# Kernel tuning notes

Measured on AMD Instinct MI355X. Metric: run time of the kernel, lower is better.

The kernel has to match this reference:

```python
import jax, jax.numpy as jnp
import numpy as np

# Problem-size constants (match input_specs / init_kwargs)
B, D, H, W = 2, 128, 128, 128   # batch and spatial grid
N = 200_000                      # number of active (non-empty) voxels
CI, CO, K = 64, 64, 3            # channels and cubic kernel size
DIL = 1                          # dilation


def setup_inputs() -> dict:
    key = jax.random.key(0)
    k1, k2, k3 = jax.random.split(key, 3)
    # Unique active voxel coordinates (submanifold conv assumes unique sites).
    rng = np.random.default_rng(0)
    lin = rng.choice(B * D * H * W, size=N, replace=False)
    b, rem = np.divmod(lin, D * H * W)
    z, rem = np.divmod(rem, H * W)
    y, x = np.divmod(rem, W)
    coords = jnp.asarray(np.stack([b, z, y, x], axis=1).astype(np.int32))  # [N,4]
    feats = jax.random.normal(k1, (N, CI), dtype=jnp.float32)
    # kaiming-uniform-ish init, layout [Co, Kd, Kh, Kw, Ci] as in the module
    fan_in = CI * K * K * K
    bound = 1.0 / np.sqrt(fan_in)
    weight = jax.random.uniform(k2, (CO, K, K, K, CI), dtype=jnp.float32,
                                minval=-bound, maxval=bound)
    bias = jax.random.uniform(k3, (CO,), dtype=jnp.float32,
                              minval=-bound, maxval=bound)
    return {"feats": feats, "weight": weight, "bias": bias, "coords": coords}


def _build_grid(coords):
    """Dense voxel hash: linear cell id -> row index in feats (-1 if empty)."""
    n = coords.shape[0]
    lin = ((coords[:, 0] * D + coords[:, 1]) * H + coords[:, 2]) * W + coords[:, 3]
    grid = jnp.full((B * D * H * W,), -1, dtype=jnp.int32)
    return grid.at[lin].set(jnp.arange(n, dtype=jnp.int32))


def reference(feats, weight, bias, coords):
    # Submanifold sparse 3D conv: out[p] = bias + sum_k W[k] @ feats[p + dil*(k - center)]
    # (only where the neighbor voxel is active; output sites == input sites).
    n = feats.shape[0]
    grid = _build_grid(coords)
    c = K // 2
    bz, z0, y0, x0 = coords[:, 0], coords[:, 1], coords[:, 2], coords[:, 3]
    out = jnp.broadcast_to(bias.astype(feats.dtype), (n, CO))
    for kd in range(K):
        for kh in range(K):
            for kw in range(K):
                dz, dy, dx = DIL * (kd - c), DIL * (kh - c), DIL * (kw - c)
                nz, ny, nx = z0 + dz, y0 + dy, x0 + dx
                inb = (nz >= 0) & (nz < D) & (ny >= 0) & (ny < H) & (nx >= 0) & (nx < W)
                nlin = ((bz * D + jnp.clip(nz, 0, D - 1)) * H
                        + jnp.clip(ny, 0, H - 1)) * W + jnp.clip(nx, 0, W - 1)
                nidx = jnp.where(inb, grid[nlin], -1)          # rulebook for this offset
                valid = (nidx >= 0)[:, None]
                g = jnp.where(valid, feats[jnp.clip(nidx, 0)], 0.0)  # gather [N,Ci]
                out = out + jnp.einsum('nc,oc->no', g, weight[:, kd, kh, kw, :])
    return out
```

## Files before the change

### kernel.cpp

```cpp
#include <hip/hip_runtime.h>
#include <hip/hip_bf16.h>

#define BDIM 2
#define DDIM 128
#define HDIM 128
#define WDIM 128
#define CI 64
#define CO 64
#define NTAPS 27
#define GRID_CELLS (BDIM * DDIM * HDIM * WDIM)
#define NCBLK (GRID_CELLS / 256)

typedef __attribute__((ext_vector_type(8))) short short8;
typedef __attribute__((ext_vector_type(4))) float floatx4;

#define WT_OFF   ((size_t)16 << 20)
#define BCNT_OFF (WT_OFF + ((size_t)256 << 10))
#define ORD_OFF  (BCNT_OFF + ((size_t)64 << 10))

__device__ __forceinline__ unsigned short f2bf(float f) {
    unsigned int u = __float_as_uint(f);
    return (unsigned short)((u + 0x7FFFu + ((u >> 16) & 1u)) >> 16);
}

__global__ __launch_bounds__(256) void scatter_kernel(
    const int* __restrict__ coords, int* __restrict__ grid, int n) {
    int i = blockIdx.x * blockDim.x + threadIdx.x;
    if (i >= n) return;
    int4 c = ((const int4*)coords)[i];
    grid[((c.x * DDIM + c.y) * HDIM + c.z) * WDIM + c.w] = i;
}

__global__ __launch_bounds__(256) void wfrag_kernel(
    const float* __restrict__ weight, short8* __restrict__ wt8) {
    int idx = blockIdx.x * blockDim.x + threadIdx.x;
    if (idx >= NTAPS * 2 * 4 * 64) return;
    int l = idx & 63, ot = (idx >> 6) & 3, s = (idx >> 8) & 1, t = idx >> 9;
    int o = ot * 16 + (l & 15);
    int k0 = s * 32 + ((l >> 4) << 3);
    const float* src = weight + ((size_t)o * NTAPS + t) * CI + k0;
    short8 v;
#pragma unroll
    for (int j = 0; j < 8; ++j) v[j] = (short)f2bf(src[j]);
    wt8[idx] = v;
}

__global__ __launch_bounds__(256) void count_kernel(
    const int* __restrict__ grid, int* __restrict__ bcnt) {
    int i = blockIdx.x * 256 + threadIdx.x;
    unsigned long long b = __ballot(grid[i] >= 0);
    __shared__ int wc[4];
    if ((threadIdx.x & 63) == 0) wc[threadIdx.x >> 6] = __popcll(b);
    __syncthreads();
    if (threadIdx.x == 0) bcnt[blockIdx.x] = wc[0] + wc[1] + wc[2] + wc[3];
}

__global__ __launch_bounds__(1024) void scan_kernel(int* __restrict__ bcnt) {
    __shared__ int part[1024];
    int tid = threadIdx.x;
    int v[16], s = 0;
#pragma unroll
    for (int k = 0; k < 16; ++k) { v[k] = bcnt[tid * 16 + k]; s += v[k]; }
    part[tid] = s;
    __syncthreads();
    for (int off = 1; off < 1024; off <<= 1) {
        int t = (tid >= off) ? part[tid - off] : 0;
        __syncthreads();
        part[tid] += t;
        __syncthreads();
    }
    int ex = tid ? part[tid - 1] : 0;
#pragma unroll
    for (int k = 0; k < 16; ++k) { int nv = ex; ex += v[k]; bcnt[tid * 16 + k] = nv; }
}

__global__ __launch_bounds__(256) void emit_kernel(
    const int* __restrict__ grid, const int* __restrict__ boff,
    int* __restrict__ order) {
    int i = blockIdx.x * 256 + threadIdx.x;
    int v = grid[i];
    int lane = threadIdx.x & 63, w = threadIdx.x >> 6;
    unsigned long long b = __ballot(v >= 0);
    __shared__ int wc[4];
    if (lane == 0) wc[w] = __popcll(b);
    __syncthreads();
    int woff = 0;
    for (int k = 0; k < w; ++k) woff += wc[k];
    if (v >= 0) {
        int rank = __popcll(b & ((1ull << lane) - 1ull));
        order[boff[blockIdx.x] + woff + rank] = v;
    }
}

__global__ __launch_bounds__(256) void conv_kernel(
    const float* __restrict__ feats, const short8* __restrict__ wt8,
    const float* __restrict__ bias, const int* __restrict__ coords,
    const int* __restrict__ grid, const int* __restrict__ order,
    float* __restrict__ out, int n) {
    __shared__ short8 bs[3][512];
    int tid = threadIdx.x;
    int w = tid >> 6, l = tid & 63, quad = l >> 4, m = l & 15;
    int jrow = blockIdx.x * 64 + w * 16 + m;
    int j = jrow < n ? jrow : n - 1;
    int p = order[j];
    int4 c = ((const int4*)coords)[p];

    int pr[7];
#pragma unroll
    for (int i = 0; i < 7; ++i) {
        int t = 4 * i + quad;
        int v = -1;
        if (t < NTAPS) {
            int dz = t / 9 - 1, rem = t % 9;
            int dy = rem / 3 - 1, dx = rem % 3 - 1;
            int nz = c.y + dz, ny = c.z + dy, nx = c.w + dx;
            if (nz >= 0 && nz < DDIM && ny >= 0 && ny < HDIM &&
                nx >= 0 && nx < WDIM)
                v = grid[((c.x * DDIM + nz) * HDIM + ny) * WDIM + nx];
        }
        pr[i] = v;
    }

    floatx4 acc0 = {0.f, 0.f, 0.f, 0.f}, acc1 = acc0, acc2 = acc0, acc3 = acc0;
    float4 xA[4], xB[4];
    int vA = -1, vB = -1;

#define STAGE(t)                                                     \
    {                                                                \
        const short8* src = wt8 + (size_t)(t) * 512 + tid * 2;       \
        short8 s0 = src[0], s1 = src[1];                             \
        bs[(t) % 3][tid * 2] = s0;                                   \
        bs[(t) % 3][tid * 2 + 1] = s1;                               \
    }

#define GATHER(t, g, vv)                                             \
    {                                                                \
        int vsrc = pr[(t) >> 2];                                     \
        vv = __shfl(vsrc, (((t) & 3) << 4) | m);                     \
        g[0] = g[1] = g[2] = g[3] = float4{0.f, 0.f, 0.f, 0.f};      \
        if (vv >= 0) {                                               \
            const float4* ar =                                       \
                (const float4*)(feats + (size_t)vv * CI + quad * 8); \
            g[0] = ar[0]; g[1] = ar[1]; g[2] = ar[8]; g[3] = ar[9];  \
        }                                                            \
    }

#define COMPUTE(t, g, vv)                                                          \
    if (__ballot(vv >= 0) != 0ull) {                                               \
        union { short8 s; __hip_bfloat162 h[4]; } f0, f1;                          \
        f0.h[0] = __float22bfloat162_rn({g[0].x, g[0].y});                         \
        f0.h[1] = __float22bfloat162_rn({g[0].z, g[0].w});                         \
        f0.h[2] = __float22bfloat162_rn({g[1].x, g[1].y});                         \
        f0.h[3] = __float22bfloat162_rn({g[1].z, g[1].w});                         \
        f1.h[0] = __float22bfloat162_rn({g[2].x, g[2].y});                         \
        f1.h[1] = __float22bfloat162_rn({g[2].z, g[2].w});                         \
        f1.h[2] = __float22bfloat162_rn({g[3].x, g[3].y});                         \
        f1.h[3] = __float22bfloat162_rn({g[3].z, g[3].w});                         \
        const short8* wb = &bs[(t) % 3][l];                                        \
        acc0 = __builtin_amdgcn_mfma_f32_16x16x32_bf16(f0.s, wb[0 * 64], acc0, 0, 0, 0); \
        acc1 = __builtin_amdgcn_mfma_f32_16x16x32_bf16(f0.s, wb[1 * 64], acc1, 0, 0, 0); \
        acc2 = __builtin_amdgcn_mfma_f32_16x16x32_bf16(f0.s, wb[2 * 64], acc2, 0, 0, 0); \
        acc3 = __builtin_amdgcn_mfma_f32_16x16x32_bf16(f0.s, wb[3 * 64], acc3, 0, 0, 0); \
        acc0 = __builtin_amdgcn_mfma_f32_16x16x32_bf16(f1.s, wb[4 * 64], acc0, 0, 0, 0); \
        acc1 = __builtin_amdgcn_mfma_f32_16x16x32_bf16(f1.s, wb[5 * 64], acc1, 0, 0, 0); \
        acc2 = __builtin_amdgcn_mfma_f32_16x16x32_bf16(f1.s, wb[6 * 64], acc2, 0, 0, 0); \
        acc3 = __builtin_amdgcn_mfma_f32_16x16x32_bf16(f1.s, wb[7 * 64], acc3, 0, 0, 0); \
    }

    STAGE(0);
    GATHER(0, xA, vA);
#pragma unroll
    for (int t = 0; t < NTAPS; ++t) {
        if (t + 1 < NTAPS) {
            STAGE(t + 1);
            if (t & 1) { GATHER(t + 1, xA, vA); } else { GATHER(t + 1, xB, vB); }
        }
        __syncthreads();
        if (t & 1) { COMPUTE(t, xB, vB); } else { COMPUTE(t, xA, vA); }
    }

    float b0 = bias[m], b1 = bias[m + 16], b2 = bias[m + 32], b3 = bias[m + 48];
#pragma unroll
    for (int r = 0; r < 4; ++r) {
        int row = quad * 4 + r;
        int jr = blockIdx.x * 64 + w * 16 + row;
        int prow = __shfl(p, row);
        if (jr < n) {
            float* orow = out + (size_t)prow * CO;
            orow[m]      = acc0[r] + b0;
            orow[m + 16] = acc1[r] + b1;
            orow[m + 32] = acc2[r] + b2;
            orow[m + 48] = acc3[r] + b3;
        }
    }
#undef STAGE
#undef GATHER
#undef COMPUTE
}

extern "C" void kernel_launch(void* const* d_in, const int* in_sizes, int n_in,
                              void* d_out, int out_size, void* d_ws, size_t ws_size,
                              hipStream_t stream) {
    const float* feats  = (const float*)d_in[0];
    const float* weight = (const float*)d_in[1];
    const float* bias   = (const float*)d_in[2];
    const int*   coords = (const int*)d_in[3];
    float* out = (float*)d_out;
    int n = in_sizes[3] / 4;

    int*    grid  = (int*)d_ws;
    short8* wt8   = (short8*)((char*)d_ws + WT_OFF);
    int*    bcnt  = (int*)((char*)d_ws + BCNT_OFF);
    int*    order = (int*)((char*)d_ws + ORD_OFF);

    (void)hipMemsetAsync(grid, 0xFF, (size_t)GRID_CELLS * sizeof(int), stream);
    scatter_kernel<<<(n + 255) / 256, 256, 0, stream>>>(coords, grid, n);
    wfrag_kernel<<<(NTAPS * 2 * 4 * 64 + 255) / 256, 256, 0, stream>>>(weight, wt8);
    count_kernel<<<NCBLK, 256, 0, stream>>>(grid, bcnt);
    scan_kernel<<<1, 1024, 0, stream>>>(bcnt);
    emit_kernel<<<NCBLK, 256, 0, stream>>>(grid, bcnt, order);
    conv_kernel<<<(n + 63) / 64, 256, 0, stream>>>(
        feats, wt8, bias, coords, grid, order, out, n);
}
```

Baseline: 194.5 us.

## Deepen conv pipeline with direct global-to-LDS weight loads and explicit waitcnt

Switches the conv kernel's tap loop from double- to triple-buffered prefetch (two taps ahead), staging weight fragments with global_load_lds instead of going through registers. It controls synchronisation with explicit vmcnt waits and raw barriers, and raises wave priority around the MFMA block. Invalid-neighbour gathers now read a shared zeroed row instead of branching. The scatter and weight-conversion kernels are merged into one setup launch. The cost is more registers and hand-tuned waitcnt counts that must match the number of issued loads.

```diff
diff --git a/kernel.cpp b/kernel.cpp
--- a/kernel.cpp
+++ b/kernel.cpp
@@ -17,32 +17,40 @@
 #define WT_OFF   ((size_t)16 << 20)
 #define BCNT_OFF (WT_OFF + ((size_t)256 << 10))
 #define ORD_OFF  (BCNT_OFF + ((size_t)64 << 10))
+#define ZROW_OFF (ORD_OFF + ((size_t)1 << 20))
+
+typedef const __attribute__((address_space(1))) void* gas_t;
+typedef __attribute__((address_space(3))) void* las_t;
 
 __device__ __forceinline__ unsigned short f2bf(float f) {
     unsigned int u = __float_as_uint(f);
     return (unsigned short)((u + 0x7FFFu + ((u >> 16) & 1u)) >> 16);
 }
 
-__global__ __launch_bounds__(256) void scatter_kernel(
-    const int* __restrict__ coords, int* __restrict__ grid, int n) {
-    int i = blockIdx.x * blockDim.x + threadIdx.x;
-    if (i >= n) return;
-    int4 c = ((const int4*)coords)[i];
-    grid[((c.x * DDIM + c.y) * HDIM + c.z) * WDIM + c.w] = i;
-}
-
-__global__ __launch_bounds__(256) void wfrag_kernel(
-    const float* __restrict__ weight, short8* __restrict__ wt8) {
-    int idx = blockIdx.x * blockDim.x + threadIdx.x;
-    if (idx >= NTAPS * 2 * 4 * 64) return;
-    int l = idx & 63, ot = (idx >> 6) & 3, s = (idx >> 8) & 1, t = idx >> 9;
-    int o = ot * 16 + (l & 15);
-    int k0 = s * 32 + ((l >> 4) << 3);
-    const float* src = weight + ((size_t)o * NTAPS + t) * CI + k0;
-    short8 v;
-#pragma unroll
-    for (int j = 0; j < 8; ++j) v[j] = (short)f2bf(src[j]);
-    wt8[idx] = v;
+__global__ __launch_bounds__(256) void setup_kernel(
+    const int* __restrict__ coords, int* __restrict__ grid, int n,
+    const float* __restrict__ weight, short8* __restrict__ wt8,
+    float* __restrict__ zrow) {
+    int bid = blockIdx.x, tid = threadIdx.x;
+    if (bid < 54) {
+        int idx = bid * 256 + tid;
+        int l = idx & 63, ot = (idx >> 6) & 3, s = (idx >> 8) & 1, t = idx >> 9;
+        int o = ot * 16 + (l & 15);
+        int k0 = s * 32 + ((l >> 4) << 3);
+        const float* src = weight + ((size_t)o * NTAPS + t) * CI + k0;
+        short8 v;
+#pragma unroll
+        for (int j = 0; j < 8; ++j) v[j] = (short)f2bf(src[j]);
+        wt8[idx] = v;
+    } else if (bid == 54) {
+        if (tid < 64) zrow[tid] = 0.f;
+    } else {
+        int i = (bid - 55) * 256 + tid;
+        if (i < n) {
+            int4 c = ((const int4*)coords)[i];
+            grid[((c.x * DDIM + c.y) * HDIM + c.z) * WDIM + c.w] = i;
+        }
+    }
 }
 
 __global__ __launch_bounds__(256) void count_kernel(
@@ -96,10 +104,13 @@
     const float* __restrict__ feats, const short8* __restrict__ wt8,
     const float* __restrict__ bias, const int* __restrict__ coords,
     const int* __restrict__ grid, const int* __restrict__ order,
-    float* __restrict__ out, int n) {
+    const float* __restrict__ zrow, float* __restrict__ out, int n) {
     __shared__ short8 bs[3][512];
     int tid = threadIdx.x;
     int w = tid >> 6, l = tid & 63, quad = l >> 4, m = l & 15;
+
+    float b0 = bias[m], b1 = bias[m + 16], b2 = bias[m + 32], b3 = bias[m + 48];
+
     int jrow = blockIdx.x * 64 + w * 16 + m;
     int j = jrow < n ? jrow : n - 1;
     int p = order[j];
@@ -122,31 +133,34 @@
     }
 
     floatx4 acc0 = {0.f, 0.f, 0.f, 0.f}, acc1 = acc0, acc2 = acc0, acc3 = acc0;
-    float4 xA[4], xB[4];
-    int vA = -1, vB = -1;
-
-#define STAGE(t)                                                     \
-    {                                                                \
-        const short8* src = wt8 + (size_t)(t) * 512 + tid * 2;       \
-        short8 s0 = src[0], s1 = src[1];                             \
-        bs[(t) % 3][tid * 2] = s0;                                   \
-        bs[(t) % 3][tid * 2 + 1] = s1;                               \
-    }
-
-#define GATHER(t, g, vv)                                             \
-    {                                                                \
-        int vsrc = pr[(t) >> 2];                                     \
-        vv = __shfl(vsrc, (((t) & 3) << 4) | m);                     \
-        g[0] = g[1] = g[2] = g[3] = float4{0.f, 0.f, 0.f, 0.f};      \
-        if (vv >= 0) {                                               \
-            const float4* ar =                                       \
-                (const float4*)(feats + (size_t)vv * CI + quad * 8); \
-            g[0] = ar[0]; g[1] = ar[1]; g[2] = ar[8]; g[3] = ar[9];  \
-        }                                                            \
-    }
-
-#define COMPUTE(t, g, vv)                                                          \
-    if (__ballot(vv >= 0) != 0ull) {                                               \
+    float4 x[3][4];
+    int vval[3];
+
+#define VMW(N) asm volatile("s_waitcnt vmcnt(" #N ")" ::: "memory")
+
+#define STAGE(t)                                                              \
+    {                                                                         \
+        const short8* gsrc = wt8 + (size_t)(t) * 512 + w * 128 + l;           \
+        __builtin_amdgcn_global_load_lds((gas_t)gsrc,                         \
+            (las_t)&bs[(t) % 3][w * 128], 16, 0, 0);                          \
+        __builtin_amdgcn_global_load_lds((gas_t)(gsrc + 64),                  \
+            (las_t)&bs[(t) % 3][w * 128 + 64], 16, 0, 0);                     \
+    }
+
+#define GATHER(t)                                                             \
+    {                                                                         \
+        int vv = __shfl(pr[(t) >> 2], (((t) & 3) << 4) | m);                  \
+        vval[(t) % 3] = vv;                                                   \
+        const float4* ar =                                                    \
+            (const float4*)(vv >= 0 ? feats + (size_t)vv * CI : zrow) +       \
+            quad * 2;                                                         \
+        float4* xb = x[(t) % 3];                                              \
+        xb[0] = ar[0]; xb[1] = ar[1]; xb[2] = ar[8]; xb[3] = ar[9];           \
+    }
+
+#define COMPUTE(t)                                                                 \
+    if (__ballot(vval[(t) % 3] >= 0) != 0ull) {                                    \
+        const float4* g = x[(t) % 3];                                              \
         union { short8 s; __hip_bfloat162 h[4]; } f0, f1;                          \
         f0.h[0] = __float22bfloat162_rn({g[0].x, g[0].y});                         \
         f0.h[1] = __float22bfloat162_rn({g[0].z, g[0].w});                         \
@@ -157,6 +171,7 @@
         f1.h[2] = __float22bfloat162_rn({g[3].x, g[3].y});                         \
         f1.h[3] = __float22bfloat162_rn({g[3].z, g[3].w});                         \
         const short8* wb = &bs[(t) % 3][l];                                        \
+        __builtin_amdgcn_s_setprio(1);                                             \
         acc0 = __builtin_amdgcn_mfma_f32_16x16x32_bf16(f0.s, wb[0 * 64], acc0, 0, 0, 0); \
         acc1 = __builtin_amdgcn_mfma_f32_16x16x32_bf16(f0.s, wb[1 * 64], acc1, 0, 0, 0); \
         acc2 = __builtin_amdgcn_mfma_f32_16x16x32_bf16(f0.s, wb[2 * 64], acc2, 0, 0, 0); \
@@ -165,21 +180,26 @@
         acc1 = __builtin_amdgcn_mfma_f32_16x16x32_bf16(f1.s, wb[5 * 64], acc1, 0, 0, 0); \
         acc2 = __builtin_amdgcn_mfma_f32_16x16x32_bf16(f1.s, wb[6 * 64], acc2, 0, 0, 0); \
         acc3 = __builtin_amdgcn_mfma_f32_16x16x32_bf16(f1.s, wb[7 * 64], acc3, 0, 0, 0); \
-    }
-
-    STAGE(0);
-    GATHER(0, xA, vA);
+        __builtin_amdgcn_s_setprio(0);                                             \
+    }
+
+    STAGE(0); GATHER(0);
+    STAGE(1); GATHER(1);
+
 #pragma unroll
     for (int t = 0; t < NTAPS; ++t) {
-        if (t + 1 < NTAPS) {
-            STAGE(t + 1);
-            if (t & 1) { GATHER(t + 1, xA, vA); } else { GATHER(t + 1, xB, vB); }
-        }
-        __syncthreads();
-        if (t & 1) { COMPUTE(t, xB, vB); } else { COMPUTE(t, xA, vA); }
-    }
-
-    float b0 = bias[m], b1 = bias[m + 16], b2 = bias[m + 32], b3 = bias[m + 48];
+        if (t + 2 < NTAPS) { STAGE(t + 2); GATHER(t + 2); }
+        if (t < NTAPS - 2)       { VMW(12); }
+        else if (t == NTAPS - 2) { VMW(6); }
+        else                     { VMW(0); }
+        __builtin_amdgcn_sched_barrier(0);
+        __builtin_amdgcn_s_barrier();
+        __builtin_amdgcn_sched_barrier(0);
+        COMPUTE(t);
+        __builtin_amdgcn_sched_barrier(0);
+        __builtin_amdgcn_s_barrier();
+    }
+
 #pragma unroll
     for (int r = 0; r < 4; ++r) {
         int row = quad * 4 + r;
@@ -196,6 +216,7 @@
 #undef STAGE
 #undef GATHER
 #undef COMPUTE
+#undef VMW
 }
 
 extern "C" void kernel_launch(void* const* d_in, const int* in_sizes, int n_in,
@@ -212,13 +233,14 @@
     short8* wt8   = (short8*)((char*)d_ws + WT_OFF);
     int*    bcnt  = (int*)((char*)d_ws + BCNT_OFF);
     int*    order = (int*)((char*)d_ws + ORD_OFF);
+    float*  zrow  = (float*)((char*)d_ws + ZROW_OFF);
 
     (void)hipMemsetAsync(grid, 0xFF, (size_t)GRID_CELLS * sizeof(int), stream);
-    scatter_kernel<<<(n + 255) / 256, 256, 0, stream>>>(coords, grid, n);
-    wfrag_kernel<<<(NTAPS * 2 * 4 * 64 + 255) / 256, 256, 0, stream>>>(weight, wt8);
+    setup_kernel<<<55 + (n + 255) / 256, 256, 0, stream>>>(
+        coords, grid, n, weight, wt8, zrow);
     count_kernel<<<NCBLK, 256, 0, stream>>>(grid, bcnt);
     scan_kernel<<<1, 1024, 0, stream>>>(bcnt);
     emit_kernel<<<NCBLK, 256, 0, stream>>>(grid, bcnt, order);
     conv_kernel<<<(n + 63) / 64, 256, 0, stream>>>(
-        feats, wt8, bias, coords, grid, order, out, n);
-}
+        feats, wt8, bias, coords, grid, order, zrow, out, n);
+}
```

Result: slower. 205.9 us (+5.8%).
